# Optimization experiments

Hardware: AMD Instinct MI355X
Metric: run time of the kernel (lower is better)

## Reference

```python
import jax, jax.numpy as jnp
import numpy as np

B, S, D = 64, 2048, 512
N_FINE = 16
MAX_SPANS = 512


def setup_inputs() -> dict:
    key = jax.random.key(0)
    k1, k2, k3 = jax.random.split(key, 3)
    hidden_layers = jax.random.normal(k1, (B, S, D), dtype=jnp.float32)
    slot_embs = jax.random.normal(k2, (D, N_FINE), dtype=jnp.float32)
    # BIO-style coarse tag ids; 1 == B tag, 2 == I tag, others = O / other coarse tags
    bin_labels = jax.random.randint(k3, (B, S), 0, 9, dtype=jnp.int32)
    return {
        "hidden_layers": hidden_layers,
        "slot_embs": slot_embs,
        "bin_labels": bin_labels,
        "coarse_B_index": 1,
        "coarse_I_index": 2,
        "max_spans": MAX_SPANS,
    }


def reference(hidden_layers, slot_embs, bin_labels, coarse_B_index, coarse_I_index, max_spans):
    # Faithful to FinePredictor with enc_type not in {trs, lstm}:
    # span j feature = hidden[B_j] + sum(hidden at I-tagged positions between B_j and B_{j+1});
    # I tokens before the first B tag are dropped (original code skips them).
    # Ragged per-sample span lists are padded to [B, max_spans] (zeros for absent spans).
    bsz, seqlen, d = hidden_layers.shape
    isB = bin_labels == coarse_B_index
    isI = bin_labels == coarse_I_index
    seg = jnp.cumsum(isB.astype(jnp.int32), axis=1) - 1  # span id per token, -1 before first B
    valid = (isB | isI) & (seg >= 0) & (seg < max_spans)
    batch_off = jnp.arange(bsz, dtype=jnp.int32)[:, None] * max_spans
    dummy = bsz * max_spans  # trash segment for invalid tokens
    seg_id = jnp.where(valid, seg + batch_off, dummy)
    feats = jax.ops.segment_sum(
        hidden_layers.reshape(bsz * seqlen, d),
        seg_id.reshape(-1),
        num_segments=dummy + 1,
    )[:-1].reshape(bsz, max_spans, d)
    # score each span feature against the fine slot-name embeddings
    preds = jnp.einsum("bkd,df->bkf", feats, slot_embs)
    return preds
```

## Files before the change

kernel.cpp:

```cpp
#include <hip/hip_runtime.h>
#include <stdint.h>

#define BATCH  64
#define SEQ    2048
#define DIM    512
#define NFINE  16
#define MSPANS 512
#define STRIDE 516

__global__ __launch_bounds__(256) void build_spans_kernel(
    const int* __restrict__ labels,
    const int* __restrict__ pB, const int* __restrict__ pI,
    int* __restrict__ count, uint32_t* __restrict__ list,
    float* __restrict__ out)
{
    const int row = blockIdx.x;
    const int tid = threadIdx.x;
    const int Btag = *pB, Itag = *pI;

    float4* oz = (float4*)(out + (size_t)row * MSPANS * NFINE);
    #pragma unroll
    for (int k = 0; k < 8; ++k)
        oz[tid + k * 256] = make_float4(0.f, 0.f, 0.f, 0.f);

    const int4* lab4 = (const int4*)(labels + (size_t)row * SEQ);
    int4 a = lab4[tid * 2], b = lab4[tid * 2 + 1];
    int l[8] = {a.x, a.y, a.z, a.w, b.x, b.y, b.z, b.w};
    int cnt = 0;
    #pragma unroll
    for (int k = 0; k < 8; ++k) cnt += (l[k] == Btag);

    __shared__ int scan[256];
    __shared__ int lcount;
    if (tid == 0) lcount = 0;
    scan[tid] = cnt;
    __syncthreads();
    for (int off = 1; off < 256; off <<= 1) {
        int v = scan[tid];
        int u = (tid >= off) ? scan[tid - off] : 0;
        __syncthreads();
        scan[tid] = v + u;
        __syncthreads();
    }
    int run = (tid > 0) ? scan[tid - 1] : 0;

    uint32_t* lrow = list + (size_t)row * SEQ;
    #pragma unroll
    for (int k = 0; k < 8; ++k) {
        const int  s   = tid * 8 + k;
        const bool isb = (l[k] == Btag);
        const bool isi = (l[k] == Itag);
        run += isb;
        const int seg = run - 1;
        if ((isb | isi) && seg >= 0 && seg < MSPANS) {
            int slot = atomicAdd(&lcount, 1);
            lrow[slot] = ((uint32_t)s << 16) | (uint32_t)seg;
        }
    }
    __syncthreads();
    if (tid == 0) count[row] = lcount;
}

__global__ __launch_bounds__(512) void span_score_kernel(
    const float* __restrict__ hidden,
    const float* __restrict__ semb,
    const int* __restrict__ count,
    const uint32_t* __restrict__ list,
    float* __restrict__ out)
{
    __shared__ float sT[NFINE * STRIDE];

    for (int i = threadIdx.x; i < DIM * NFINE; i += 512)
        sT[(i & 15) * STRIDE + (i >> 4)] = semb[i];
    __syncthreads();

    const int row  = blockIdx.x >> 4;
    const int wir  = (blockIdx.x & 15) * 8 + (threadIdx.x >> 6);
    const int lane = threadIdx.x & 63;
    const int f = lane & 15, q = lane >> 4;

    const int n = count[row];
    const float*    hbase = hidden + (size_t)row * SEQ * DIM;
    float*          obase = out    + (size_t)row * MSPANS * NFINE;
    const uint32_t* lrow  = list   + (size_t)row * SEQ;
    const float4*   sv    = (const float4*)&sT[f * STRIDE + q * 128];

    for (int idx = wir; idx < n; idx += 128) {
        const uint32_t e = lrow[idx];
        const int s   = (int)(e >> 16);
        const int seg = (int)(e & 0xffff);
        const float4* h4 = (const float4*)(hbase + (size_t)s * DIM + q * 128);
        float a0 = 0.f, a1 = 0.f, a2 = 0.f, a3 = 0.f;
        #pragma unroll 8
        for (int i = 0; i < 32; ++i) {
            float4 h  = h4[i];
            float4 s4 = sv[i];
            a0 = fmaf(h.x, s4.x, a0);
            a1 = fmaf(h.y, s4.y, a1);
            a2 = fmaf(h.z, s4.z, a2);
            a3 = fmaf(h.w, s4.w, a3);
        }
        float acc = (a0 + a1) + (a2 + a3);
        acc += __shfl_xor(acc, 16);
        acc += __shfl_xor(acc, 32);
        if (q == 0) atomicAdd(obase + seg * NFINE + f, acc);
    }
}

extern "C" void kernel_launch(void* const* d_in, const int* in_sizes, int n_in,
                              void* d_out, int out_size, void* d_ws, size_t ws_size,
                              hipStream_t stream)
{
    const float* hidden = (const float*)d_in[0];
    const float* semb   = (const float*)d_in[1];
    const int*   labels = (const int*)d_in[2];
    const int*   pB     = (const int*)d_in[3];
    const int*   pI     = (const int*)d_in[4];
    float* out = (float*)d_out;

    int*      count = (int*)d_ws;
    uint32_t* list  = (uint32_t*)((char*)d_ws + 256);

    build_spans_kernel<<<BATCH, 256, 0, stream>>>(labels, pB, pI, count, list, out);
    span_score_kernel<<<BATCH * 16, 512, 0, stream>>>(hidden, semb, count, list, out);
}
```

Before: 355.4 us.

## Build ordered CSR span lists and reduce per span without atomics

The span builder now runs a second block-wide prefix scan so the token list is compacted in sequence order. It also writes a CSR-style pointer array with one start offset per span. The scoring kernel gives each wavefront a whole span and loops over that span's tokens. It writes the 16 scores with plain stores instead of issuing a float atomicAdd per token. This removes global atomic traffic, at the cost of an extra scan in the builder and a serial, variable-length token loop per wavefront that can unbalance work.

```diff
diff --git a/kernel.cpp b/kernel.cpp
--- a/kernel.cpp
+++ b/kernel.cpp
@@ -11,7 +11,9 @@
 __global__ __launch_bounds__(256) void build_spans_kernel(
     const int* __restrict__ labels,
     const int* __restrict__ pB, const int* __restrict__ pI,
-    int* __restrict__ count, uint32_t* __restrict__ list,
+    int* __restrict__ cnt,
+    int* __restrict__ spanPtr,
+    uint32_t* __restrict__ list,
     float* __restrict__ out)
 {
     const int row = blockIdx.x;
@@ -26,14 +28,13 @@
     const int4* lab4 = (const int4*)(labels + (size_t)row * SEQ);
     int4 a = lab4[tid * 2], b = lab4[tid * 2 + 1];
     int l[8] = {a.x, a.y, a.z, a.w, b.x, b.y, b.z, b.w};
-    int cnt = 0;
-    #pragma unroll
-    for (int k = 0; k < 8; ++k) cnt += (l[k] == Btag);
 
     __shared__ int scan[256];
-    __shared__ int lcount;
-    if (tid == 0) lcount = 0;
-    scan[tid] = cnt;
+
+    int bcnt = 0;
+    #pragma unroll
+    for (int k = 0; k < 8; ++k) bcnt += (l[k] == Btag);
+    scan[tid] = bcnt;
     __syncthreads();
     for (int off = 1; off < 256; off <<= 1) {
         int v = scan[tid];
@@ -42,29 +43,62 @@
         scan[tid] = v + u;
         __syncthreads();
     }
-    int run = (tid > 0) ? scan[tid - 1] : 0;
+    const int bexcl = (tid > 0) ? scan[tid - 1] : 0;
+    const int btot  = scan[255];
+    __syncthreads();
 
-    uint32_t* lrow = list + (size_t)row * SEQ;
+    int  seg8[8];
+    bool val8[8];
+    bool isb8[8];
+    int vcnt = 0, run = bexcl;
     #pragma unroll
     for (int k = 0; k < 8; ++k) {
-        const int  s   = tid * 8 + k;
         const bool isb = (l[k] == Btag);
         const bool isi = (l[k] == Itag);
         run += isb;
         const int seg = run - 1;
-        if ((isb | isi) && seg >= 0 && seg < MSPANS) {
-            int slot = atomicAdd(&lcount, 1);
-            lrow[slot] = ((uint32_t)s << 16) | (uint32_t)seg;
+        const bool v = (isb | isi) && seg >= 0 && seg < MSPANS;
+        seg8[k] = seg; val8[k] = v; isb8[k] = isb;
+        vcnt += v;
+    }
+
+    scan[tid] = vcnt;
+    __syncthreads();
+    for (int off = 1; off < 256; off <<= 1) {
+        int v = scan[tid];
+        int u = (tid >= off) ? scan[tid - off] : 0;
+        __syncthreads();
+        scan[tid] = v + u;
+        __syncthreads();
+    }
+    const int vexcl = (tid > 0) ? scan[tid - 1] : 0;
+    const int vtot  = scan[255];
+
+    uint32_t* lrow = list + (size_t)row * SEQ;
+    int* sp = spanPtr + row * (MSPANS + 1);
+    int slot = vexcl;
+    #pragma unroll
+    for (int k = 0; k < 8; ++k) {
+        if (val8[k]) {
+            const int s = tid * 8 + k;
+            lrow[slot] = ((uint32_t)s << 16) | (uint32_t)seg8[k];
+            if (isb8[k]) sp[seg8[k]] = slot;
+            ++slot;
         }
     }
-    __syncthreads();
-    if (tid == 0) count[row] = lcount;
+    if (tid == 0) {
+        const int nsp = (btot < MSPANS) ? btot : MSPANS;
+        cnt[row]      = vtot;
+        cnt[64 + row] = nsp;
+        sp[nsp]       = vtot;
+    }
 }
 
 __global__ __launch_bounds__(512) void span_score_kernel(
     const float* __restrict__ hidden,
     const float* __restrict__ semb,
-    const int* __restrict__ count,
+    const int* __restrict__ cnt,
+    const int* __restrict__ spanPtr,
     const uint32_t* __restrict__ list,
     float* __restrict__ out)
 {
@@ -79,31 +113,33 @@
     const int lane = threadIdx.x & 63;
     const int f = lane & 15, q = lane >> 4;
 
-    const int n = count[row];
-    const float*    hbase = hidden + (size_t)row * SEQ * DIM;
-    float*          obase = out    + (size_t)row * MSPANS * NFINE;
-    const uint32_t* lrow  = list   + (size_t)row * SEQ;
+    const int nsp = cnt[64 + row];
+    const float*    hbase = hidden  + (size_t)row * SEQ * DIM;
+    float*          obase = out     + (size_t)row * MSPANS * NFINE;
+    const uint32_t* lrow  = list    + (size_t)row * SEQ;
+    const int*      sp    = spanPtr + row * (MSPANS + 1);
     const float4*   sv    = (const float4*)&sT[f * STRIDE + q * 128];
 
-    for (int idx = wir; idx < n; idx += 128) {
-        const uint32_t e = lrow[idx];
-        const int s   = (int)(e >> 16);
-        const int seg = (int)(e & 0xffff);
-        const float4* h4 = (const float4*)(hbase + (size_t)s * DIM + q * 128);
+    for (int seg = wir; seg < nsp; seg += 128) {
+        const int i0 = sp[seg], i1 = sp[seg + 1];
         float a0 = 0.f, a1 = 0.f, a2 = 0.f, a3 = 0.f;
-        #pragma unroll 8
-        for (int i = 0; i < 32; ++i) {
-            float4 h  = h4[i];
-            float4 s4 = sv[i];
-            a0 = fmaf(h.x, s4.x, a0);
-            a1 = fmaf(h.y, s4.y, a1);
-            a2 = fmaf(h.z, s4.z, a2);
-            a3 = fmaf(h.w, s4.w, a3);
+        for (int i = i0; i < i1; ++i) {
+            const int s = (int)(lrow[i] >> 16);
+            const float4* h4 = (const float4*)(hbase + (size_t)s * DIM + q * 128);
+            #pragma unroll 8
+            for (int j = 0; j < 32; ++j) {
+                float4 h  = h4[j];
+                float4 s4 = sv[j];
+                a0 = fmaf(h.x, s4.x, a0);
+                a1 = fmaf(h.y, s4.y, a1);
+                a2 = fmaf(h.z, s4.z, a2);
+                a3 = fmaf(h.w, s4.w, a3);
+            }
         }
         float acc = (a0 + a1) + (a2 + a3);
         acc += __shfl_xor(acc, 16);
         acc += __shfl_xor(acc, 32);
-        if (q == 0) atomicAdd(obase + seg * NFINE + f, acc);
+        if (lane < NFINE) obase[seg * NFINE + lane] = acc;
     }
 }
 
@@ -118,9 +154,10 @@
     const int*   pI     = (const int*)d_in[4];
     float* out = (float*)d_out;
 
-    int*      count = (int*)d_ws;
-    uint32_t* list  = (uint32_t*)((char*)d_ws + 256);
+    int*      cnt     = (int*)d_ws;
+    int*      spanPtr = (int*)((char*)d_ws + 512);
+    uint32_t* list    = (uint32_t*)((char*)d_ws + 131840);
 
-    build_spans_kernel<<<BATCH, 256, 0, stream>>>(labels, pB, pI, count, list, out);
-    span_score_kernel<<<BATCH * 16, 512, 0, stream>>>(hidden, semb, count, list, out);
+    build_spans_kernel<<<BATCH, 256, 0, stream>>>(labels, pB, pI, cnt, spanPtr, list, out);
+    span_score_kernel<<<BATCH * 16, 512, 0, stream>>>(hidden, semb, cnt, spanPtr, list, out);
 }
```

Measured after the change: 383.3 us. 1.08x slower.
